# Optimization experiments

Measured on AMD Instinct MI355X. Metric: run time of the kernel, lower is better.

## Reference

```python
import jax, jax.numpy as jnp
import numpy as np
import math

INF = 10000000000.0
D_KEY = 64


def setup_inputs() -> dict:
    key = jax.random.key(0)
    kq, kk, kv = jax.random.split(key, 3)
    B, S, D = 4, 4096, D_KEY
    return {
        "query": jax.random.normal(kq, (B, S, D), dtype=jnp.float32),
        "key": jax.random.normal(kk, (B, S, D), dtype=jnp.float32),
        "value": jax.random.normal(kv, (B, S, D), dtype=jnp.float32),
    }


def reference(query, key, value):
    # dot_products: [B, Sq, Sk]
    scale = math.sqrt(D_KEY)
    scores = jnp.einsum("bqd,bkd->bqk", query, key)
    S = key.shape[1]
    # causal: subtract INF on strict upper triangle (triu(1)), before scaling
    tri = jnp.triu(jnp.full((S, S), INF, dtype=scores.dtype), k=1)
    scores = scores - tri[None, :, :]
    logits = scores / scale
    probs = jax.nn.softmax(logits, axis=-1)  # softmax over key dim
    # dropout p=0.0 -> identity
    return jnp.einsum("bqk,bkd->bqd", probs, value)
```

## Files before the change

kernel.cpp:

```cpp
#include <hip/hip_runtime.h>
#include <hip/hip_bf16.h>
#include <math.h>

#define B_  4
#define S_  4096
#define D_  64
#define NQT 64
#define NST 32
#define QSC 0.18033688f
#define M0  20.0f

typedef __attribute__((ext_vector_type(8))) short bf16x8;
typedef __attribute__((ext_vector_type(4))) float f32x4;
typedef __attribute__((ext_vector_type(4))) short short4v;

static __device__ inline short f2bf(float f) {
    union { float f; unsigned u; } v; v.f = f;
    unsigned u = v.u;
    unsigned r = u + 0x7fff + ((u >> 16) & 1);
    return (short)(r >> 16);
}
static __device__ inline float bf2f(short s) {
    union { unsigned u; float f; } v; v.u = ((unsigned)(unsigned short)s) << 16;
    return v.f;
}
static __device__ inline unsigned cvt_pk_bf16(float lo, float hi) {
    unsigned r;
    asm("v_cvt_pk_bf16_f32 %0, %1, %2" : "=v"(r) : "v"(lo), "v"(hi));
    return r;
}

__global__ __launch_bounds__(256) void fa_prep(const float* __restrict__ K,
                                               const float* __restrict__ V,
                                               short* __restrict__ Kbf,
                                               short* __restrict__ Vtbf)
{
    const int b   = blockIdx.x >> 6;
    const int st  = blockIdx.x & 63;
    const int tid = threadIdx.x;
    __shared__ short Vs[64 * 72];

    const size_t tbase = ((size_t)b * S_ + (size_t)st * 64) * D_;
    #pragma unroll
    for (int rr = 0; rr < 4; ++rr) {
        int i = tid + rr * 256;
        size_t e = tbase + (size_t)i * 4;
        f32x4 k = *(const f32x4*)(K + e);
        union { short4v s; unsigned u[2]; } ks;
        ks.u[0] = cvt_pk_bf16(k[0], k[1]);
        ks.u[1] = cvt_pk_bf16(k[2], k[3]);
        *(short4v*)(Kbf + e) = ks.s;
        f32x4 v = *(const f32x4*)(V + e);
        int key = i >> 4, d4 = (i & 15) * 4;
        int slot = (key & 32) + (((key & 15) >> 2) << 3) + (((key >> 4) & 1) << 2) + (key & 3);
        Vs[(d4 + 0) * 72 + slot] = f2bf(v[0]);
        Vs[(d4 + 1) * 72 + slot] = f2bf(v[1]);
        Vs[(d4 + 2) * 72 + slot] = f2bf(v[2]);
        Vs[(d4 + 3) * 72 + slot] = f2bf(v[3]);
    }
    __syncthreads();
    #pragma unroll
    for (int cc = 0; cc < 2; ++cc) {
        int c = tid + cc * 256;
        int d = c >> 3, sg = c & 7;
        bf16x8 row = *(const bf16x8*)&Vs[d * 72 + sg * 8];
        *(bf16x8*)(Vtbf + ((size_t)(b * D_ + d)) * S_ + (size_t)st * 64 + sg * 8) = row;
    }
}

__global__ __launch_bounds__(512, 6) void fa_part(const float* __restrict__ Qf,
                                               const short* __restrict__ Kbf,
                                               const short* __restrict__ Vtbf,
                                               short* __restrict__ Opart,
                                               float* __restrict__ Lpart,
                                               int CH, int T)
{
    const int bid = blockIdx.x;
    const int b   = bid / T;
    int r = bid - b * T;
    int qt2 = NST - 1;
    while (true) {
        int n = (2 * qt2 + 2 + CH - 1) / CH;
        if (r < n) break;
        r -= n; --qt2;
    }
    const int kt0 = r * CH;
    const int nkt = 2 * qt2 + 2;
    const int kt1 = (kt0 + CH < nkt) ? kt0 + CH : nkt;

    const int tid  = threadIdx.x;
    const int wave = tid >> 6;
    const int lane = tid & 63;
    const int lm   = lane & 15;
    const int lk   = lane >> 4;

    __shared__ __align__(16) short Ks[2][64 * 64];
    __shared__ __align__(16) short Vt[2][64 * 64];

    bf16x8 qA[2];
    {
        const float* qp = Qf + ((size_t)(b * S_ + qt2 * 128 + wave * 16 + lm)) * D_;
        #pragma unroll
        for (int h = 0; h < 2; ++h) {
            f32x4 a0 = *(const f32x4*)(qp + h * 32 + lk * 8);
            f32x4 a1 = *(const f32x4*)(qp + h * 32 + lk * 8 + 4);
            union { bf16x8 v; unsigned u[4]; } qa;
            qa.u[0] = cvt_pk_bf16(a0[0] * QSC, a0[1] * QSC);
            qa.u[1] = cvt_pk_bf16(a0[2] * QSC, a0[3] * QSC);
            qa.u[2] = cvt_pk_bf16(a1[0] * QSC, a1[1] * QSC);
            qa.u[3] = cvt_pk_bf16(a1[2] * QSC, a1[3] * QSC);
            qA[h] = qa.v;
        }
    }

    bf16x8 onesF;
    #pragma unroll
    for (int j = 0; j < 8; ++j) onesF[j] = (short)0x3F80;

    const int srow = tid >> 3;
    const int sseg = (tid & 7) ^ (srow & 7);
    const char* kgp = (const char*)(Kbf + (size_t)b * S_ * D_)
                    + (size_t)(kt0 * 64 + srow) * 128 + sseg * 16;
    const char* vgp = (const char*)(Vtbf + ((size_t)(b * D_ + srow)) * S_)
                    + (size_t)kt0 * 128 + sseg * 16;

    bf16x8 kreg = *(const bf16x8*)kgp;
    bf16x8 vreg = *(const bf16x8*)vgp;
    kgp += 8192; vgp += 128;
    *(bf16x8*)&Ks[0][tid * 8] = kreg;
    *(bf16x8*)&Vt[0][tid * 8] = vreg;
    __syncthreads();
    if (kt0 + 1 < kt1) {
        kreg = *(const bf16x8*)kgp;
        vreg = *(const bf16x8*)vgp;
        kgp += 8192; vgp += 128;
    }

    f32x4 l4 = (f32x4){0.f, 0.f, 0.f, 0.f};
    f32x4 o_acc[4];
    #pragma unroll
    for (int dt = 0; dt < 4; ++dt) o_acc[dt] = (f32x4){0.f, 0.f, 0.f, 0.f};

    const int wrow = wave * 16 + lk * 4;
    const int qrow = wave * 16 + lm;
    int cur = 0;

    for (int kt = kt0; kt < kt1; ++kt) {
        f32x4 s4[4];
        __builtin_amdgcn_s_setprio(1);
        #pragma unroll
        for (int ct = 0; ct < 4; ++ct) {
            f32x4 acc = (f32x4){-M0, -M0, -M0, -M0};
            #pragma unroll
            for (int h = 0; h < 2; ++h) {
                int seg = (h * 4 + lk) ^ (lm & 7);
                bf16x8 kF = *(const bf16x8*)&Ks[cur][(ct * 16 + lm) * 64 + seg * 8];
                acc = __builtin_amdgcn_mfma_f32_16x16x32_bf16(kF, qA[h], acc, 0, 0, 0);
            }
            s4[ct] = acc;
        }
        __builtin_amdgcn_s_setprio(0);

        if (kt >= 2 * qt2) {
            const int koff = kt * 64 - qt2 * 128 + lk * 4;
            #pragma unroll
            for (int ct = 0; ct < 4; ++ct) {
                #pragma unroll
                for (int rr = 0; rr < 4; ++rr) {
                    if (koff + ct * 16 + rr > qrow) s4[ct][rr] = -INFINITY;
                }
            }
        }

        #pragma unroll
        for (int ct = 0; ct < 4; ++ct) {
            #pragma unroll
            for (int rr = 0; rr < 4; ++rr) s4[ct][rr] = exp2f(s4[ct][rr]);
        }
        bf16x8 aF[2];
        #pragma unroll
        for (int kh = 0; kh < 2; ++kh) {
            union { bf16x8 v; unsigned u[4]; } pa;
            pa.u[0] = cvt_pk_bf16(s4[2 * kh][0],     s4[2 * kh][1]);
            pa.u[1] = cvt_pk_bf16(s4[2 * kh][2],     s4[2 * kh][3]);
            pa.u[2] = cvt_pk_bf16(s4[2 * kh + 1][0], s4[2 * kh + 1][1]);
            pa.u[3] = cvt_pk_bf16(s4[2 * kh + 1][2], s4[2 * kh + 1][3]);
            aF[kh] = pa.v;
        }
        __builtin_amdgcn_s_setprio(1);
        #pragma unroll
        for (int kh = 0; kh < 2; ++kh)
            l4 = __builtin_amdgcn_mfma_f32_16x16x32_bf16(aF[kh], onesF, l4, 0, 0, 0);
        #pragma unroll
        for (int dt = 0; dt < 4; ++dt) {
            #pragma unroll
            for (int kh = 0; kh < 2; ++kh) {
                int seg = (kh * 4 + lk) ^ (lm & 7);
                bf16x8 bF = *(const bf16x8*)&Vt[cur][(dt * 16 + lm) * 64 + seg * 8];
                o_acc[dt] = __builtin_amdgcn_mfma_f32_16x16x32_bf16(aF[kh], bF, o_acc[dt], 0, 0, 0);
            }
        }
        __builtin_amdgcn_s_setprio(0);

        if (kt + 1 < kt1) {
            *(bf16x8*)&Ks[cur ^ 1][tid * 8] = kreg;
            *(bf16x8*)&Vt[cur ^ 1][tid * 8] = vreg;
            __syncthreads();
            if (kt + 2 < kt1) {
                kreg = *(const bf16x8*)kgp;
                vreg = *(const bf16x8*)vgp;
                kgp += 8192; vgp += 128;
            }
            cur ^= 1;
        }
    }

    short* Op = Opart + (size_t)bid * (128 * D_);
    if (lm == 0) {
        #pragma unroll
        for (int rr = 0; rr < 4; ++rr)
            Lpart[(size_t)bid * 128 + wrow + rr] = l4[rr];
    }
    #pragma unroll
    for (int dt = 0; dt < 4; ++dt) {
        unsigned o01 = cvt_pk_bf16(o_acc[dt][0], o_acc[dt][1]);
        unsigned o23 = cvt_pk_bf16(o_acc[dt][2], o_acc[dt][3]);
        Op[(wrow + 0) * D_ + dt * 16 + lm] = (short)(o01 & 0xffff);
        Op[(wrow + 1) * D_ + dt * 16 + lm] = (short)(o01 >> 16);
        Op[(wrow + 2) * D_ + dt * 16 + lm] = (short)(o23 & 0xffff);
        Op[(wrow + 3) * D_ + dt * 16 + lm] = (short)(o23 >> 16);
    }
}

__global__ __launch_bounds__(256) void fa_combine(const short* __restrict__ Opart,
                                                  const float* __restrict__ Lpart,
                                                  float* __restrict__ O,
                                                  int CH, int T)
{
    const int idx = blockIdx.x * 256 + threadIdx.x;
    const int b   = idx / (S_ * 16);
    const int rem = idx - b * (S_ * 16);
    const int q   = rem >> 4;
    const int d4  = (rem & 15) << 2;
    const int qt2 = q >> 7;
    const int rit = q & 127;

    int F = 0;
    for (int y = qt2 + 1; y < NST; ++y) F += (2 * y + 2 + CH - 1) / CH;
    const int base = b * T + F;
    const int nch  = (2 * qt2 + 2 + CH - 1) / CH;

    float L = 0.f;
    f32x4 acc = (f32x4){0.f, 0.f, 0.f, 0.f};
    for (int c = 0; c < nch; ++c) {
        L += Lpart[(size_t)(base + c) * 128 + rit];
        short4v o = *(const short4v*)(Opart + (size_t)(base + c) * (128 * D_) + rit * D_ + d4);
        acc[0] += bf2f(o[0]); acc[1] += bf2f(o[1]);
        acc[2] += bf2f(o[2]); acc[3] += bf2f(o[3]);
    }
    float inv = 1.f / L;
    f32x4 outv;
    outv[0] = acc[0] * inv; outv[1] = acc[1] * inv;
    outv[2] = acc[2] * inv; outv[3] = acc[3] * inv;
    *(f32x4*)(O + (size_t)idx * 4) = outv;
}

__global__ __launch_bounds__(256) void fa_fwd(const float* __restrict__ Q,
                                              const float* __restrict__ K,
                                              const float* __restrict__ V,
                                              float* __restrict__ O)
{
    const int qt   = (gridDim.x - 1) - blockIdx.x;
    const int b    = blockIdx.y;
    const int tid  = threadIdx.x;
    const int wave = tid >> 6;
    const int lane = tid & 63;
    const int lm   = lane & 15;
    const int lk   = lane >> 4;

    __shared__ short Ks[64 * 72];
    __shared__ short Vt[64 * 72];
    __shared__ short Ps[64 * 72];

    const float* Qb = Q + ((size_t)b * S_ + (size_t)qt * 64) * D_;
    const float* Kb = K + (size_t)b * S_ * D_;
    const float* Vb = V + (size_t)b * S_ * D_;

    bf16x8 qA[2];
    {
        const float* qp = Qb + (wave * 16 + lm) * D_;
        #pragma unroll
        for (int h = 0; h < 2; ++h) {
            const float* p = qp + h * 32 + lk * 8;
            #pragma unroll
            for (int j = 0; j < 8; ++j) qA[h][j] = f2bf(p[j] * 0.125f);
        }
    }
    float m_i[4], l_i[4];
    f32x4 o_acc[4];
    #pragma unroll
    for (int rr = 0; rr < 4; ++rr) { m_i[rr] = -INFINITY; l_i[rr] = 0.f; }
    #pragma unroll
    for (int dt = 0; dt < 4; ++dt) o_acc[dt] = (f32x4){0.f, 0.f, 0.f, 0.f};

    const int n_kt = qt + 1;
    for (int kt = 0; kt < n_kt; ++kt) {
        __syncthreads();
        #pragma unroll
        for (int rr = 0; rr < 4; ++rr) {
            int i   = tid + rr * 256;
            int row = i >> 4;
            int c4  = (i & 15) * 4;
            const size_t gbase = ((size_t)(kt * 64 + row)) * D_ + c4;
            f32x4 kv = *(const f32x4*)(Kb + gbase);
            short4v ks;
            ks[0] = f2bf(kv[0]); ks[1] = f2bf(kv[1]);
            ks[2] = f2bf(kv[2]); ks[3] = f2bf(kv[3]);
            *(short4v*)&Ks[row * 72 + c4] = ks;
            f32x4 vv = *(const f32x4*)(Vb + gbase);
            Vt[(c4 + 0) * 72 + row] = f2bf(vv[0]);
            Vt[(c4 + 1) * 72 + row] = f2bf(vv[1]);
            Vt[(c4 + 2) * 72 + row] = f2bf(vv[2]);
            Vt[(c4 + 3) * 72 + row] = f2bf(vv[3]);
        }
        __syncthreads();
        f32x4 s4[4];
        #pragma unroll
        for (int ct = 0; ct < 4; ++ct) {
            f32x4 acc = (f32x4){0.f, 0.f, 0.f, 0.f};
            #pragma unroll
            for (int h = 0; h < 2; ++h) {
                bf16x8 bF = *(const bf16x8*)&Ks[(ct * 16 + lm) * 72 + h * 32 + lk * 8];
                acc = __builtin_amdgcn_mfma_f32_16x16x32_bf16(qA[h], bF, acc, 0, 0, 0);
            }
            s4[ct] = acc;
        }
        if (kt == qt) {
            #pragma unroll
            for (int ct = 0; ct < 4; ++ct) {
                #pragma unroll
                for (int rr = 0; rr < 4; ++rr) {
                    int qrow = wave * 16 + lk * 4 + rr;
                    int kcol = ct * 16 + lm;
                    if (kcol > qrow) s4[ct][rr] = -INFINITY;
                }
            }
        }
        float alpha[4];
        #pragma unroll
        for (int rr = 0; rr < 4; ++rr) {
            float mx = fmaxf(fmaxf(s4[0][rr], s4[1][rr]), fmaxf(s4[2][rr], s4[3][rr]));
            mx = fmaxf(mx, __shfl_xor(mx, 1));
            mx = fmaxf(mx, __shfl_xor(mx, 2));
            mx = fmaxf(mx, __shfl_xor(mx, 4));
            mx = fmaxf(mx, __shfl_xor(mx, 8));
            float mn = fmaxf(m_i[rr], mx);
            alpha[rr] = __expf(m_i[rr] - mn);
            m_i[rr] = mn;
        }
        float rsum[4] = {0.f, 0.f, 0.f, 0.f};
        #pragma unroll
        for (int ct = 0; ct < 4; ++ct) {
            #pragma unroll
            for (int rr = 0; rr < 4; ++rr) {
                float p = __expf(s4[ct][rr] - m_i[rr]);
                s4[ct][rr] = p;
                rsum[rr] += p;
            }
        }
        #pragma unroll
        for (int rr = 0; rr < 4; ++rr) {
            float rs = rsum[rr];
            rs += __shfl_xor(rs, 1);
            rs += __shfl_xor(rs, 2);
            rs += __shfl_xor(rs, 4);
            rs += __shfl_xor(rs, 8);
            l_i[rr] = l_i[rr] * alpha[rr] + rs;
        }
        #pragma unroll
        for (int ct = 0; ct < 4; ++ct) {
            #pragma unroll
            for (int rr = 0; rr < 4; ++rr) {
                Ps[(wave * 16 + lk * 4 + rr) * 72 + ct * 16 + lm] = f2bf(s4[ct][rr]);
            }
        }
        #pragma unroll
        for (int dt = 0; dt < 4; ++dt) {
            #pragma unroll
            for (int rr = 0; rr < 4; ++rr) o_acc[dt][rr] *= alpha[rr];
        }
        #pragma unroll
        for (int dt = 0; dt < 4; ++dt) {
            #pragma unroll
            for (int kh = 0; kh < 2; ++kh) {
                bf16x8 aF = *(const bf16x8*)&Ps[(wave * 16 + lm) * 72 + kh * 32 + lk * 8];
                bf16x8 bF = *(const bf16x8*)&Vt[(dt * 16 + lm) * 72 + kh * 32 + lk * 8];
                o_acc[dt] = __builtin_amdgcn_mfma_f32_16x16x32_bf16(aF, bF, o_acc[dt], 0, 0, 0);
            }
        }
    }
    float* Ob = O + ((size_t)b * S_ + (size_t)qt * 64) * D_;
    #pragma unroll
    for (int rr = 0; rr < 4; ++rr) {
        float inv = 1.f / l_i[rr];
        int row = wave * 16 + lk * 4 + rr;
        #pragma unroll
        for (int dt = 0; dt < 4; ++dt) {
            Ob[row * D_ + dt * 16 + lm] = o_acc[dt][rr] * inv;
        }
    }
}

extern "C" void kernel_launch(void* const* d_in, const int* in_sizes, int n_in,
                              void* d_out, int out_size, void* d_ws, size_t ws_size,
                              hipStream_t stream) {
    const float* Q = (const float*)d_in[0];
    const float* K = (const float*)d_in[1];
    const float* V = (const float*)d_in[2];
    float* O = (float*)d_out;

    const size_t convShorts = (size_t)B_ * S_ * D_;
    int CH = 0, T = 0;
    const int chs[5] = {6, 8, 16, 32, 64};
    for (int k = 0; k < 5; ++k) {
        int c = chs[k];
        int t = 0;
        for (int q2 = 0; q2 < NST; ++q2) t += (2 * q2 + 2 + c - 1) / c;
        size_t need = 2 * convShorts * 2
                    + (size_t)B_ * t * (128 * D_) * 2
                    + (size_t)B_ * t * 128 * 4;
        if (need <= ws_size) { CH = c; T = t; break; }
    }
    if (CH == 0) {
        dim3 grid(NQT, B_);
        fa_fwd<<<grid, 256, 0, stream>>>(Q, K, V, O);
        return;
    }
    short* Kbf   = (short*)d_ws;
    short* Vtbf  = Kbf + convShorts;
    short* Opart = Vtbf + convShorts;
    float* Lpart = (float*)(Opart + (size_t)B_ * T * (128 * D_));

    fa_prep<<<dim3(B_ * NQT), 256, 0, stream>>>(K, V, Kbf, Vtbf);
    fa_part<<<dim3(B_ * T), 512, 0, stream>>>(Q, Kbf, Vtbf, Opart, Lpart, CH, T);
    fa_combine<<<dim3((B_ * S_ * 16) / 256), 256, 0, stream>>>(Opart, Lpart, O, CH, T);
}
```

Baseline: 93.45 us.

## Load K/V tiles straight into LDS with global_load_lds and pre-swizzle in prep

The prep kernel now writes K and transposed V in global memory already XOR-swizzled, so each thread's 16-byte chunk lands in the correct LDS slot. The attention kernel then uses global_load_lds (direct global-to-LDS DMA) for double-buffered K/V tiles, issued at the top of each iteration. This removes the register staging and the separate LDS stores, freeing VGPRs. The risk is that the hardware's per-wave LDS placement may not match the assumed wave*512 offset, and correctness depends on the implicit wait before the barrier.

```diff
diff --git a/kernel.cpp b/kernel.cpp
--- a/kernel.cpp
+++ b/kernel.cpp
@@ -28,6 +28,12 @@
     unsigned r;
     asm("v_cvt_pk_bf16_f32 %0, %1, %2" : "=v"(r) : "v"(lo), "v"(hi));
     return r;
+}
+static __device__ inline void gload_lds16(const void* g, void* l) {
+    __builtin_amdgcn_global_load_lds(
+        (const __attribute__((address_space(1))) unsigned int*)g,
+        (__attribute__((address_space(3))) unsigned int*)l,
+        16, 0, 0);
 }
 
 __global__ __launch_bounds__(256) void fa_prep(const float* __restrict__ K,
@@ -49,9 +55,10 @@
         union { short4v s; unsigned u[2]; } ks;
         ks.u[0] = cvt_pk_bf16(k[0], k[1]);
         ks.u[1] = cvt_pk_bf16(k[2], k[3]);
-        *(short4v*)(Kbf + e) = ks.s;
+        int key = i >> 4, d4 = (i & 15) * 4;
+        int d4s = (((d4 >> 3) ^ (key & 7)) << 3) + (d4 & 7);
+        *(short4v*)(Kbf + tbase + (size_t)key * 64 + d4s) = ks.s;
         f32x4 v = *(const f32x4*)(V + e);
-        int key = i >> 4, d4 = (i & 15) * 4;
         int slot = (key & 32) + (((key & 15) >> 2) << 3) + (((key >> 4) & 1) << 2) + (key & 3);
         Vs[(d4 + 0) * 72 + slot] = f2bf(v[0]);
         Vs[(d4 + 1) * 72 + slot] = f2bf(v[1]);
@@ -64,7 +71,7 @@
         int c = tid + cc * 256;
         int d = c >> 3, sg = c & 7;
         bf16x8 row = *(const bf16x8*)&Vs[d * 72 + sg * 8];
-        *(bf16x8*)(Vtbf + ((size_t)(b * D_ + d)) * S_ + (size_t)st * 64 + sg * 8) = row;
+        *(bf16x8*)(Vtbf + ((size_t)(b * D_ + d)) * S_ + (size_t)st * 64 + (sg ^ (d & 7)) * 8) = row;
     }
 }
 
@@ -117,24 +124,15 @@
     #pragma unroll
     for (int j = 0; j < 8; ++j) onesF[j] = (short)0x3F80;
 
-    const int srow = tid >> 3;
-    const int sseg = (tid & 7) ^ (srow & 7);
     const char* kgp = (const char*)(Kbf + (size_t)b * S_ * D_)
-                    + (size_t)(kt0 * 64 + srow) * 128 + sseg * 16;
-    const char* vgp = (const char*)(Vtbf + ((size_t)(b * D_ + srow)) * S_)
-                    + (size_t)kt0 * 128 + sseg * 16;
-
-    bf16x8 kreg = *(const bf16x8*)kgp;
-    bf16x8 vreg = *(const bf16x8*)vgp;
+                    + (size_t)kt0 * 8192 + tid * 16;
+    const char* vgp = (const char*)(Vtbf + ((size_t)(b * D_ + (tid >> 3))) * S_)
+                    + (size_t)kt0 * 128 + (tid & 7) * 16;
+
+    gload_lds16(kgp, &Ks[0][wave * 512]);
+    gload_lds16(vgp, &Vt[0][wave * 512]);
     kgp += 8192; vgp += 128;
-    *(bf16x8*)&Ks[0][tid * 8] = kreg;
-    *(bf16x8*)&Vt[0][tid * 8] = vreg;
     __syncthreads();
-    if (kt0 + 1 < kt1) {
-        kreg = *(const bf16x8*)kgp;
-        vreg = *(const bf16x8*)vgp;
-        kgp += 8192; vgp += 128;
-    }
 
     f32x4 l4 = (f32x4){0.f, 0.f, 0.f, 0.f};
     f32x4 o_acc[4];
@@ -146,6 +144,12 @@
     int cur = 0;
 
     for (int kt = kt0; kt < kt1; ++kt) {
+        if (kt + 1 < kt1) {
+            gload_lds16(kgp, &Ks[cur ^ 1][wave * 512]);
+            gload_lds16(vgp, &Vt[cur ^ 1][wave * 512]);
+            kgp += 8192; vgp += 128;
+        }
+
         f32x4 s4[4];
         __builtin_amdgcn_s_setprio(1);
         #pragma unroll
@@ -203,14 +207,7 @@
         __builtin_amdgcn_s_setprio(0);
 
         if (kt + 1 < kt1) {
-            *(bf16x8*)&Ks[cur ^ 1][tid * 8] = kreg;
-            *(bf16x8*)&Vt[cur ^ 1][tid * 8] = vreg;
             __syncthreads();
-            if (kt + 2 < kt1) {
-                kreg = *(const bf16x8*)kgp;
-                vreg = *(const bf16x8*)vgp;
-                kgp += 8192; vgp += 128;
-            }
             cur ^= 1;
         }
     }
```

Result: no change. 94.69 us (+1.3%).
